# Kernel tuning notes

Hardware: AMD Instinct MI355X
Metric: run time of the kernel (lower is better)

Reference implementation:

```python
import jax, jax.numpy as jnp
import numpy as np

B = 4096
D_IN = 1024
H1 = 2048
H2 = 1024
E = 7          # num_experts, forced by broadcasting in source
T = 2          # num_tasks
NS = 7         # scene dimension of S
EMB_ROWS = 10
EMB_DIM = 16


def setup_inputs() -> dict:
    key = jax.random.key(0)
    ks = jax.random.split(key, 8)
    x = jax.random.normal(ks[0], (B, D_IN), dtype=jnp.float32)
    scene = jax.random.randint(ks[1], (B,), 0, E)
    # Expert MLP params, stacked over experts: Linear(D_IN->H1)+ReLU, Linear(H1->H2)+ReLU
    W1 = jax.random.normal(ks[2], (E, D_IN, H1), dtype=jnp.float32) * (1.0 / np.sqrt(D_IN))
    b1 = jnp.zeros((E, H1), dtype=jnp.float32)
    W2 = jax.random.normal(ks[3], (E, H1, H2), dtype=jnp.float32) * (1.0 / np.sqrt(H1))
    b2 = jnp.zeros((E, H2), dtype=jnp.float32)
    # Routing tensor S: [7, input_dim+16, num_experts] (xavier-like init)
    S = jax.random.normal(ks[4], (NS, D_IN + EMB_DIM, E), dtype=jnp.float32) * 0.02
    scene_emb = jax.random.normal(ks[5], (EMB_ROWS, EMB_DIM), dtype=jnp.float32)
    return {"x": x, "scene": scene, "W1": W1, "b1": b1, "W2": W2, "b2": b2,
            "S": S, "scene_emb": scene_emb}


def _forward(x, scene, W1, b1, W2, b2, S, scene_emb):
    # Experts (vectorized over the E expert MLPs): [B,E,H2]
    h = jax.nn.relu(jnp.einsum('bd,edh->beh', x, W1) + b1)
    experts_out = jax.nn.relu(jnp.einsum('beh,eho->beo', h, W2) + b2)

    se = scene_emb[scene]                       # [B,16]
    xc = jnp.concatenate([x, se], axis=-1)      # [B, D_IN+16]
    G = jnp.einsum('bd,sde->bse', xc, S)        # [B, 7, E]
    G = jnp.transpose(G, (0, 2, 1))             # [B, E, 7]
    G = jax.nn.softmax(G, axis=-1)

    logG = jnp.log(G)                           # [B, E, 7]
    q = jnp.sum(jnp.log(G * 7.0) / 7.0, axis=-1)  # [B, E]

    KG = jnp.eye(E, dtype=x.dtype)
    ses = KG[scene][:, None, :]                 # [B, 1, E]

    _, pi = jax.lax.top_k(jnp.sum(ses * logG, axis=-1), 6)  # [B,6]
    _, qi = jax.lax.top_k(q, 6)                              # [B,6]
    select = ((KG[pi].sum(axis=1) + KG[qi].sum(axis=1)) > 0).astype(x.dtype)  # [B,E]

    gate = jax.nn.softmax(jnp.sum(G * ses, axis=-1), axis=-1) * select  # [B,E]
    out = jnp.einsum('be,bed->bd', gate, experts_out)                    # [B,H2]
    # self.gate ModuleList is unused in the source forward; each task output is identical
    return jnp.stack([out] * T, axis=0)         # [T, B, H2]


def reference(x, scene, W1, b1, W2, b2, S, scene_emb):
    return _forward(x, scene, W1, b1, W2, b2, S, scene_emb)
```

## Files before the change

kernel.cpp:

```cpp
#include <hip/hip_runtime.h>
#include <hip/hip_bf16.h>

typedef unsigned short u16;
typedef __bf16 bf8 __attribute__((ext_vector_type(8)));
typedef float f4 __attribute__((ext_vector_type(4)));

__device__ __forceinline__ u16 f2bf(float f) {
    unsigned int u = __float_as_uint(f);
    u = (u + 0x7fffu + ((u >> 16) & 1u)) >> 16;
    return (u16)u;
}

__device__ __forceinline__ void gload16(const u16* g, u16* l) {
    __builtin_amdgcn_global_load_lds((const __attribute__((address_space(1))) void*)g,
                                     (__attribute__((address_space(3))) void*)l, 16, 0, 0);
}

__global__ void cvt_x_kernel(const float* __restrict__ in, u16* __restrict__ out, int n4) {
    int i = blockIdx.x * blockDim.x + threadIdx.x;
    int stride = gridDim.x * blockDim.x;
    for (; i < n4; i += stride) {
        float4 v = ((const float4*)in)[i];
        ushort4 o;
        o.x = f2bf(v.x); o.y = f2bf(v.y); o.z = f2bf(v.z); o.w = f2bf(v.w);
        ((ushort4*)out)[i] = o;
    }
}

__global__ void transpose_cvt_kernel(const float* __restrict__ in, u16* __restrict__ out,
                                     int R, int C) {
    __shared__ float t[32][33];
    int e = blockIdx.z;
    int c0 = blockIdx.x * 32, r0 = blockIdx.y * 32;
    int tx = threadIdx.x & 31, ty = threadIdx.x >> 5;
    const float* ip = in + (size_t)e * R * C;
    u16* op = out + (size_t)e * R * C;
#pragma unroll
    for (int k = 0; k < 32; k += 8)
        t[ty + k][tx] = ip[(size_t)(r0 + ty + k) * C + c0 + tx];
    __syncthreads();
#pragma unroll
    for (int k = 0; k < 32; k += 8)
        op[(size_t)(c0 + ty + k) * R + r0 + tx] = f2bf(t[tx][ty + k]);
}

__global__ void transpose_S_kernel(const float* __restrict__ S, float* __restrict__ ST) {
    int idx = blockIdx.x * 256 + threadIdx.x;
    if (idx >= 1040 * 52) return;
    int d = idx / 52, c = idx % 52;
    ST[idx] = (c < 49) ? S[(c / 7) * 7280 + d * 7 + (c % 7)] : 0.f;
}

__global__ void gating_kernel(const float* __restrict__ x, const int* __restrict__ scene,
                              const float* __restrict__ ST, const float* __restrict__ semb,
                              float* __restrict__ gate) {
    __shared__ float xc[4][1040];
    __shared__ float Lsh[4][49];
    int wv = threadIdx.x >> 6, lane = threadIdx.x & 63;
    int row = blockIdx.x * 4 + wv;
    float* xcw = xc[wv];
    const float* xr = x + (size_t)row * 1024;
    for (int d = lane; d < 1024; d += 64) xcw[d] = xr[d];
    int sc = scene[row];
    if (lane < 16) xcw[1024 + lane] = semb[sc * 16 + lane];
    __syncthreads();

    if (lane < 49) {
        const float* STp = ST + lane;
        float a0 = 0.f, a1 = 0.f, a2 = 0.f, a3 = 0.f;
        for (int d = 0; d < 1040; d += 4) {
            a0 += xcw[d]     * STp[d * 52];
            a1 += xcw[d + 1] * STp[d * 52 + 52];
            a2 += xcw[d + 2] * STp[d * 52 + 104];
            a3 += xcw[d + 3] * STp[d * 52 + 156];
        }
        Lsh[wv][lane] = (a0 + a1) + (a2 + a3);
    }
    __syncthreads();

    if (lane == 0) {
        float logG[7][7], Gsc[7], piS[7], qS[7];
        for (int e = 0; e < 7; e++) {
            float L[7];
            float m = -1e30f;
            for (int s = 0; s < 7; s++) { L[s] = Lsh[wv][s * 7 + e]; m = fmaxf(m, L[s]); }
            float sum = 0.f;
            for (int s = 0; s < 7; s++) sum += expf(L[s] - m);
            float lse = m + logf(sum);
            float qs = 0.f;
            for (int s = 0; s < 7; s++) { logG[e][s] = L[s] - lse; qs += logG[e][s]; }
            piS[e] = logG[e][sc];
            qS[e] = qs;
            Gsc[e] = expf(logG[e][sc]);
        }
        int epi = 0, eqi = 0; float bp = piS[0], bq = qS[0];
        for (int e = 1; e < 7; e++) {
            if (piS[e] <= bp) { bp = piS[e]; epi = e; }
            if (qS[e]  <= bq) { bq = qS[e];  eqi = e; }
        }
        float mg = -1e30f;
        for (int e = 0; e < 7; e++) mg = fmaxf(mg, Gsc[e]);
        float sum = 0.f;
        float ex[7];
        for (int e = 0; e < 7; e++) { ex[e] = expf(Gsc[e] - mg); sum += ex[e]; }
        float inv = 1.f / sum;
        for (int e = 0; e < 7; e++) {
            float g = ex[e] * inv;
            if (e == epi && e == eqi) g = 0.f;
            gate[row * 7 + e] = g;
        }
    }
}

__global__ __launch_bounds__(256, 2) void gemm1_kernel(
    const u16* __restrict__ A, const u16* __restrict__ BT,
    const float* __restrict__ b1, u16* __restrict__ H) {
    const int M = 4096, K = 1024, N = 2048;
    int e = blockIdx.z;
    int bm = blockIdx.y, bn = blockIdx.x;
    __shared__ __align__(16) u16 As[128 * 32];
    __shared__ __align__(16) u16 Bs[128 * 32];
    int tid = threadIdx.x, lane = tid & 63, w = tid >> 6;
    int wm = w >> 1, wn = w & 1;

    const u16* Ag = A + (size_t)(bm * 128 + (tid >> 2)) * K + (tid & 3) * 8;
    const u16* Bg = BT + (size_t)e * N * K + (size_t)(bn * 128 + (tid >> 2)) * K + (tid & 3) * 8;

    f4 acc[4][4] = {};
    int arow = lane & 15, kch = (lane >> 4) * 8;
    const u16* Asr = As + (wm * 64 + arow) * 32 + kch;
    const u16* Bsr = Bs + (wn * 64 + arow) * 32 + kch;

    for (int kt = 0; kt < K; kt += 32) {
        gload16(Ag + kt,           As + tid * 8);
        gload16(Ag + kt + 64 * K,  As + tid * 8 + 64 * 32);
        gload16(Bg + kt,           Bs + tid * 8);
        gload16(Bg + kt + 64 * K,  Bs + tid * 8 + 64 * 32);
        __syncthreads();
        bf8 a[4], b[4];
#pragma unroll
        for (int mi = 0; mi < 4; mi++) a[mi] = *(const bf8*)(Asr + mi * 16 * 32);
#pragma unroll
        for (int ni = 0; ni < 4; ni++) b[ni] = *(const bf8*)(Bsr + ni * 16 * 32);
#pragma unroll
        for (int mi = 0; mi < 4; mi++)
#pragma unroll
            for (int ni = 0; ni < 4; ni++)
                acc[mi][ni] = __builtin_amdgcn_mfma_f32_16x16x32_bf16(a[mi], b[ni], acc[mi][ni], 0, 0, 0);
        __syncthreads();
    }

    int cn0 = bn * 128 + wn * 64 + (lane & 15);
    int rm0 = bm * 128 + wm * 64 + (lane >> 4) * 4;
    float bias[4];
#pragma unroll
    for (int ni = 0; ni < 4; ni++) bias[ni] = b1[e * N + cn0 + ni * 16];
    u16* Hp = H + (size_t)e * M * N;
#pragma unroll
    for (int mi = 0; mi < 4; mi++)
#pragma unroll
        for (int i = 0; i < 4; i++) {
            size_t rbase = (size_t)(rm0 + mi * 16 + i) * N;
#pragma unroll
            for (int ni = 0; ni < 4; ni++) {
                float v = acc[mi][ni][i] + bias[ni];
                Hp[rbase + cn0 + ni * 16] = f2bf(fmaxf(v, 0.f));
            }
        }
}

__global__ __launch_bounds__(256, 2) void gemm2_kernel(
    const u16* __restrict__ H, const u16* __restrict__ W2T,
    const float* __restrict__ b2, const float* __restrict__ gate,
    float* __restrict__ part) {
    const int M = 4096, K = 2048, N = 1024;
    int id = blockIdx.x;
    int group = id >> 8;
    int id2 = id & 255;
    int bmr = id2 & 7, rest = id2 >> 3;
    int bn = rest >> 2, bmq = rest & 3;
    int bm = bmq * 8 + bmr;
    int e0 = group ? 4 : 0, e1 = group ? 7 : 4;

    __shared__ __align__(16) u16 As[128 * 32];
    __shared__ __align__(16) u16 Bs[128 * 32];
    __shared__ float gsh[128][7];
    int tid = threadIdx.x, lane = tid & 63, w = tid >> 6;
    int wm = w >> 1, wn = w & 1;

    for (int i = tid; i < 128 * 7; i += 256)
        gsh[i / 7][i % 7] = gate[(bm * 128 + i / 7) * 7 + i % 7];

    f4 fin[4][4] = {};
    int arow = lane & 15, kch = (lane >> 4) * 8;
    const u16* Asr = As + (wm * 64 + arow) * 32 + kch;
    const u16* Bsr = Bs + (wn * 64 + arow) * 32 + kch;
    int lrow0 = wm * 64 + (lane >> 4) * 4;
    int rm0 = bm * 128 + lrow0;
    int cn0 = bn * 128 + wn * 64 + (lane & 15);

    for (int e = e0; e < e1; e++) {
        const u16* Ag = H + ((size_t)e * M + bm * 128 + (tid >> 2)) * K + (tid & 3) * 8;
        const u16* Bg = W2T + ((size_t)e * N + bn * 128 + (tid >> 2)) * K + (tid & 3) * 8;
        f4 acc[4][4] = {};
        for (int kt = 0; kt < K; kt += 32) {
            gload16(Ag + kt,           As + tid * 8);
            gload16(Ag + kt + 64 * K,  As + tid * 8 + 64 * 32);
            gload16(Bg + kt,           Bs + tid * 8);
            gload16(Bg + kt + 64 * K,  Bs + tid * 8 + 64 * 32);
            __syncthreads();
            bf8 a[4], b[4];
#pragma unroll
            for (int mi = 0; mi < 4; mi++) a[mi] = *(const bf8*)(Asr + mi * 16 * 32);
#pragma unroll
            for (int ni = 0; ni < 4; ni++) b[ni] = *(const bf8*)(Bsr + ni * 16 * 32);
#pragma unroll
            for (int mi = 0; mi < 4; mi++)
#pragma unroll
                for (int ni = 0; ni < 4; ni++)
                    acc[mi][ni] = __builtin_amdgcn_mfma_f32_16x16x32_bf16(a[mi], b[ni], acc[mi][ni], 0, 0, 0);
            __syncthreads();
        }
        float bias[4];
#pragma unroll
        for (int ni = 0; ni < 4; ni++) bias[ni] = b2[e * N + cn0 + ni * 16];
#pragma unroll
        for (int mi = 0; mi < 4; mi++)
#pragma unroll
            for (int i = 0; i < 4; i++) {
                float g = gsh[lrow0 + mi * 16 + i][e];
#pragma unroll
                for (int ni = 0; ni < 4; ni++)
                    fin[mi][ni][i] += g * fmaxf(acc[mi][ni][i] + bias[ni], 0.f);
            }
    }

    float* po = part + (size_t)group * M * N;
#pragma unroll
    for (int mi = 0; mi < 4; mi++)
#pragma unroll
        for (int i = 0; i < 4; i++) {
            size_t r = (size_t)(rm0 + mi * 16 + i);
#pragma unroll
            for (int ni = 0; ni < 4; ni++)
                po[r * N + cn0 + ni * 16] = fin[mi][ni][i];
        }
}

__global__ void combine_kernel(const float* __restrict__ p0, const float* __restrict__ p1,
                               float* __restrict__ out, int n4) {
    int i = blockIdx.x * blockDim.x + threadIdx.x;
    int stride = gridDim.x * blockDim.x;
    for (; i < n4; i += stride) {
        float4 a = ((const float4*)p0)[i];
        float4 b = ((const float4*)p1)[i];
        float4 v = make_float4(a.x + b.x, a.y + b.y, a.z + b.z, a.w + b.w);
        ((float4*)out)[i] = v;
        ((float4*)out)[i + n4] = v;
    }
}

extern "C" void kernel_launch(void* const* d_in, const int* in_sizes, int n_in,
                              void* d_out, int out_size, void* d_ws, size_t ws_size,
                              hipStream_t stream) {
    const float* x     = (const float*)d_in[0];
    const int*   scene = (const int*)d_in[1];
    const float* W1    = (const float*)d_in[2];
    const float* b1    = (const float*)d_in[3];
    const float* W2    = (const float*)d_in[4];
    const float* b2    = (const float*)d_in[5];
    const float* S     = (const float*)d_in[6];
    const float* semb  = (const float*)d_in[7];
    float* out = (float*)d_out;

    char* ws = (char*)d_ws;
    float* part = (float*)(ws);
    u16*   xb   = (u16*)(ws);
    u16*   W1T  = (u16*)(ws + 8388608);
    u16*   W2T  = (u16*)(ws + 37748736);
    u16*   Hb   = (u16*)(ws + 67108864);
    float* gate = (float*)(ws + 184549376);
    float* ST   = (float*)(ws + 184664064);

    cvt_x_kernel<<<2048, 256, 0, stream>>>(x, xb, 4096 * 1024 / 4);
    transpose_cvt_kernel<<<dim3(64, 32, 7), 256, 0, stream>>>(W1, W1T, 1024, 2048);
    transpose_cvt_kernel<<<dim3(32, 64, 7), 256, 0, stream>>>(W2, W2T, 2048, 1024);
    transpose_S_kernel<<<(1040 * 52 + 255) / 256, 256, 0, stream>>>(S, ST);
    gating_kernel<<<1024, 256, 0, stream>>>(x, scene, ST, semb, gate);
    gemm1_kernel<<<dim3(16, 32, 7), 256, 0, stream>>>(xb, W1T, b1, Hb);
    gemm2_kernel<<<512, 256, 0, stream>>>(Hb, W2T, b2, gate, part);
    combine_kernel<<<2048, 256, 0, stream>>>(part, part + 4096 * 1024, out, 4096 * 1024 / 4);
}
```

Before: 425.0 us.

## Replace both expert GEMMs with double-buffered 8-wave 128x256 pipelined kernel

Replaces gemm1 and gemm2 with one templated 512-thread kernel. It uses 128x256 tiles with a K-step of 64, double-buffered LDS with an XOR swizzle, and interleaves async global-to-LDS loads with MFMA phases using explicit waitcnt, sched_barrier and setprio. The aim is to hide memory latency and cut the barrier and LDS bank-conflict overhead of the old single-buffered 128x128 loop. The gemm2 grid now uses 256 blocks with an XCD-aware mapping, which risks lower occupancy, and the hand-tuned waitcnt counts could be fragile.

```diff
diff --git a/kernel.cpp b/kernel.cpp
--- a/kernel.cpp
+++ b/kernel.cpp
@@ -112,139 +112,215 @@
     }
 }
 
-__global__ __launch_bounds__(256, 2) void gemm1_kernel(
-    const u16* __restrict__ A, const u16* __restrict__ BT,
-    const float* __restrict__ b1, u16* __restrict__ H) {
-    const int M = 4096, K = 1024, N = 2048;
-    int e = blockIdx.z;
-    int bm = blockIdx.y, bn = blockIdx.x;
-    __shared__ __align__(16) u16 As[128 * 32];
-    __shared__ __align__(16) u16 Bs[128 * 32];
-    int tid = threadIdx.x, lane = tid & 63, w = tid >> 6;
-    int wm = w >> 1, wn = w & 1;
-
-    const u16* Ag = A + (size_t)(bm * 128 + (tid >> 2)) * K + (tid & 3) * 8;
-    const u16* Bg = BT + (size_t)e * N * K + (size_t)(bn * 128 + (tid >> 2)) * K + (tid & 3) * 8;
+template<bool G2>
+__global__ __launch_bounds__(512, 2) void gemm8p_kernel(
+    const u16* __restrict__ Abase, const u16* __restrict__ Bbase,
+    const float* __restrict__ bias, const float* __restrict__ gate,
+    void* __restrict__ outp)
+{
+    constexpr int M = 4096;
+    constexpr int K = G2 ? 2048 : 1024;
+    constexpr int N = G2 ? 1024 : 2048;
+    constexpr int NT = K / 64;
+    constexpr int LOG2NT = G2 ? 5 : 4;
+
+    extern __shared__ u16 lds[];
+
+    const int tid = threadIdx.x;
+    const int lane = tid & 63;
+    const int wid = tid >> 6;
+    const int wr = wid >> 2, wc = wid & 3;
+    const int ln15 = lane & 15, lnk = (lane >> 4) * 8;
+
+    int bm, bn, e0, nE, grp;
+    if constexpr (G2) {
+        int id = blockIdx.x;
+        int xcd = id & 7, slot = id >> 3;
+        grp = xcd & 1;
+        bn = slot & 3;
+        bm = (slot >> 2) * 4 + (xcd >> 1);
+        e0 = grp * 4; nE = grp ? 3 : 4;
+    } else {
+        int id = blockIdx.x;
+        e0 = id >> 8;
+        bm = (id & 255) >> 3;
+        bn = id & 7;
+        nE = 1; grp = 0;
+    }
+    const int NTtot = nE * NT;
+
+    const int sr = tid >> 3;
+    const int sc = (tid & 7) * 8;
+
+    auto stageA = [&](int gt, int buf) {
+#pragma unroll
+        for (int l = 0; l < 2; ++l) {
+            int r = l * 64 + sr;
+            int cs = sc ^ (((r >> 2) & 1) << 4);
+            const u16* g = Abase + (G2 ? (size_t)(e0 + (gt >> LOG2NT)) * M * K : (size_t)0)
+                         + (size_t)(bm * 128 + r) * K + (gt & (NT - 1)) * 64 + cs;
+            gload16(g, lds + buf * 24576 + l * 4096 + tid * 8);
+        }
+    };
+    auto stageB = [&](int gt, int buf, int h) {
+#pragma unroll
+        for (int l = 0; l < 2; ++l) {
+            int rb = h * 128 + l * 64 + sr;
+            int cs = sc ^ (((rb >> 2) & 1) << 4);
+            const u16* g = Bbase + (size_t)(e0 + (gt >> LOG2NT)) * N * K
+                         + (size_t)(bn * 256 + rb) * K + (gt & (NT - 1)) * 64 + cs;
+            gload16(g, lds + buf * 24576 + 8192 + h * 8192 + l * 4096 + tid * 8);
+        }
+    };
+    auto aoff = [&](int mi, int ks) {
+        int r = wr * 64 + mi * 16 + ln15;
+        int c = ks * 32 + lnk;
+        return r * 64 + (c ^ (((r >> 2) & 1) << 4));
+    };
+    auto boff = [&](int ni, int ks) {
+        int rb = wc * 64 + ni * 16 + ln15;
+        int c = ks * 32 + lnk;
+        return rb * 64 + (c ^ (((rb >> 2) & 1) << 4));
+    };
 
     f4 acc[4][4] = {};
-    int arow = lane & 15, kch = (lane >> 4) * 8;
-    const u16* Asr = As + (wm * 64 + arow) * 32 + kch;
-    const u16* Bsr = Bs + (wn * 64 + arow) * 32 + kch;
-
-    for (int kt = 0; kt < K; kt += 32) {
-        gload16(Ag + kt,           As + tid * 8);
-        gload16(Ag + kt + 64 * K,  As + tid * 8 + 64 * 32);
-        gload16(Bg + kt,           Bs + tid * 8);
-        gload16(Bg + kt + 64 * K,  Bs + tid * 8 + 64 * 32);
-        __syncthreads();
-        bf8 a[4], b[4];
-#pragma unroll
-        for (int mi = 0; mi < 4; mi++) a[mi] = *(const bf8*)(Asr + mi * 16 * 32);
-#pragma unroll
-        for (int ni = 0; ni < 4; ni++) b[ni] = *(const bf8*)(Bsr + ni * 16 * 32);
-#pragma unroll
-        for (int mi = 0; mi < 4; mi++)
-#pragma unroll
-            for (int ni = 0; ni < 4; ni++)
-                acc[mi][ni] = __builtin_amdgcn_mfma_f32_16x16x32_bf16(a[mi], b[ni], acc[mi][ni], 0, 0, 0);
-        __syncthreads();
-    }
-
-    int cn0 = bn * 128 + wn * 64 + (lane & 15);
-    int rm0 = bm * 128 + wm * 64 + (lane >> 4) * 4;
-    float bias[4];
-#pragma unroll
-    for (int ni = 0; ni < 4; ni++) bias[ni] = b1[e * N + cn0 + ni * 16];
-    u16* Hp = H + (size_t)e * M * N;
-#pragma unroll
-    for (int mi = 0; mi < 4; mi++)
-#pragma unroll
-        for (int i = 0; i < 4; i++) {
-            size_t rbase = (size_t)(rm0 + mi * 16 + i) * N;
-#pragma unroll
-            for (int ni = 0; ni < 4; ni++) {
-                float v = acc[mi][ni][i] + bias[ni];
-                Hp[rbase + cn0 + ni * 16] = f2bf(fmaxf(v, 0.f));
+    f4 fin[4][4] = {};
+    bf8 aA[2][2], bL[2][2], bH[2][2];
+
+    stageA(0, 0); stageB(0, 0, 0); stageB(0, 0, 1);
+
+    for (int gt = 0; gt < NTtot; ++gt) {
+        const int cur = gt & 1, nxt = cur ^ 1;
+        const bool more = (gt + 1 < NTtot);
+        const u16* Ac = lds + cur * 24576;
+        const u16* Bc = lds + cur * 24576 + 8192;
+        if (more) {
+            stageA(gt + 1, nxt); stageB(gt + 1, nxt, 0);
+            asm volatile("s_waitcnt vmcnt(4)" ::: "memory");
+        } else {
+            asm volatile("s_waitcnt vmcnt(0)" ::: "memory");
+        }
+        __builtin_amdgcn_sched_barrier(0);
+        __builtin_amdgcn_s_barrier();
+        __builtin_amdgcn_sched_barrier(0);
+#pragma unroll
+        for (int mi = 0; mi < 2; ++mi)
+#pragma unroll
+            for (int ks = 0; ks < 2; ++ks)
+                aA[mi][ks] = *(const bf8*)(Ac + aoff(mi, ks));
+#pragma unroll
+        for (int ni = 0; ni < 2; ++ni)
+#pragma unroll
+            for (int ks = 0; ks < 2; ++ks)
+                bL[ni][ks] = *(const bf8*)(Bc + boff(ni, ks));
+        asm volatile("s_waitcnt lgkmcnt(0)" ::: "memory");
+        __builtin_amdgcn_sched_barrier(0);
+        __builtin_amdgcn_s_setprio(1);
+#pragma unroll
+        for (int mi = 0; mi < 2; ++mi)
+#pragma unroll
+            for (int ni = 0; ni < 2; ++ni)
+#pragma unroll
+                for (int ks = 0; ks < 2; ++ks)
+                    acc[mi][ni] = __builtin_amdgcn_mfma_f32_16x16x32_bf16(aA[mi][ks], bL[ni][ks], acc[mi][ni], 0, 0, 0);
+        __builtin_amdgcn_s_setprio(0);
+        if (more) stageB(gt + 1, nxt, 1);
+#pragma unroll
+        for (int ni = 0; ni < 2; ++ni)
+#pragma unroll
+            for (int ks = 0; ks < 2; ++ks)
+                bH[ni][ks] = *(const bf8*)(Bc + boff(2 + ni, ks));
+        asm volatile("s_waitcnt lgkmcnt(0)" ::: "memory");
+        __builtin_amdgcn_sched_barrier(0);
+        __builtin_amdgcn_s_setprio(1);
+#pragma unroll
+        for (int mi = 0; mi < 2; ++mi)
+#pragma unroll
+            for (int ni = 0; ni < 2; ++ni)
+#pragma unroll
+                for (int ks = 0; ks < 2; ++ks)
+                    acc[mi][2 + ni] = __builtin_amdgcn_mfma_f32_16x16x32_bf16(aA[mi][ks], bH[ni][ks], acc[mi][2 + ni], 0, 0, 0);
+        __builtin_amdgcn_s_setprio(0);
+#pragma unroll
+        for (int mi = 0; mi < 2; ++mi)
+#pragma unroll
+            for (int ks = 0; ks < 2; ++ks)
+                aA[mi][ks] = *(const bf8*)(Ac + aoff(2 + mi, ks));
+        asm volatile("s_waitcnt lgkmcnt(0)" ::: "memory");
+        __builtin_amdgcn_sched_barrier(0);
+        __builtin_amdgcn_s_setprio(1);
+#pragma unroll
+        for (int mi = 0; mi < 2; ++mi)
+#pragma unroll
+            for (int ni = 0; ni < 2; ++ni)
+#pragma unroll
+                for (int ks = 0; ks < 2; ++ks)
+                    acc[2 + mi][2 + ni] = __builtin_amdgcn_mfma_f32_16x16x32_bf16(aA[mi][ks], bH[ni][ks], acc[2 + mi][2 + ni], 0, 0, 0);
+        __builtin_amdgcn_s_setprio(0);
+        __builtin_amdgcn_sched_barrier(0);
+        __builtin_amdgcn_s_barrier();
+        __builtin_amdgcn_sched_barrier(0);
+        __builtin_amdgcn_s_setprio(1);
+#pragma unroll
+        for (int mi = 0; mi < 2; ++mi)
+#pragma unroll
+            for (int ni = 0; ni < 2; ++ni)
+#pragma unroll
+                for (int ks = 0; ks < 2; ++ks)
+                    acc[2 + mi][ni] = __builtin_amdgcn_mfma_f32_16x16x32_bf16(aA[mi][ks], bL[ni][ks], acc[2 + mi][ni], 0, 0, 0);
+        __builtin_amdgcn_s_setprio(0);
+        __builtin_amdgcn_sched_barrier(0);
+        if constexpr (G2) {
+            if ((gt & (NT - 1)) == NT - 1) {
+                int e = e0 + (gt >> LOG2NT);
+                float bloc[4];
+#pragma unroll
+                for (int ni = 0; ni < 4; ++ni)
+                    bloc[ni] = bias[e * N + bn * 256 + wc * 64 + ni * 16 + ln15];
+#pragma unroll
+                for (int mi = 0; mi < 4; ++mi)
+#pragma unroll
+                    for (int i = 0; i < 4; ++i) {
+                        int row = bm * 128 + wr * 64 + mi * 16 + (lane >> 4) * 4 + i;
+                        float g = gate[row * 7 + e];
+#pragma unroll
+                        for (int ni = 0; ni < 4; ++ni) {
+                            fin[mi][ni][i] += g * fmaxf(acc[mi][ni][i] + bloc[ni], 0.f);
+                            acc[mi][ni][i] = 0.f;
+                        }
+                    }
             }
         }
-}
-
-__global__ __launch_bounds__(256, 2) void gemm2_kernel(
-    const u16* __restrict__ H, const u16* __restrict__ W2T,
-    const float* __restrict__ b2, const float* __restrict__ gate,
-    float* __restrict__ part) {
-    const int M = 4096, K = 2048, N = 1024;
-    int id = blockIdx.x;
-    int group = id >> 8;
-    int id2 = id & 255;
-    int bmr = id2 & 7, rest = id2 >> 3;
-    int bn = rest >> 2, bmq = rest & 3;
-    int bm = bmq * 8 + bmr;
-    int e0 = group ? 4 : 0, e1 = group ? 7 : 4;
-
-    __shared__ __align__(16) u16 As[128 * 32];
-    __shared__ __align__(16) u16 Bs[128 * 32];
-    __shared__ float gsh[128][7];
-    int tid = threadIdx.x, lane = tid & 63, w = tid >> 6;
-    int wm = w >> 1, wn = w & 1;
-
-    for (int i = tid; i < 128 * 7; i += 256)
-        gsh[i / 7][i % 7] = gate[(bm * 128 + i / 7) * 7 + i % 7];
-
-    f4 fin[4][4] = {};
-    int arow = lane & 15, kch = (lane >> 4) * 8;
-    const u16* Asr = As + (wm * 64 + arow) * 32 + kch;
-    const u16* Bsr = Bs + (wn * 64 + arow) * 32 + kch;
-    int lrow0 = wm * 64 + (lane >> 4) * 4;
-    int rm0 = bm * 128 + lrow0;
-    int cn0 = bn * 128 + wn * 64 + (lane & 15);
-
-    for (int e = e0; e < e1; e++) {
-        const u16* Ag = H + ((size_t)e * M + bm * 128 + (tid >> 2)) * K + (tid & 3) * 8;
-        const u16* Bg = W2T + ((size_t)e * N + bn * 128 + (tid >> 2)) * K + (tid & 3) * 8;
-        f4 acc[4][4] = {};
-        for (int kt = 0; kt < K; kt += 32) {
-            gload16(Ag + kt,           As + tid * 8);
-            gload16(Ag + kt + 64 * K,  As + tid * 8 + 64 * 32);
-            gload16(Bg + kt,           Bs + tid * 8);
-            gload16(Bg + kt + 64 * K,  Bs + tid * 8 + 64 * 32);
-            __syncthreads();
-            bf8 a[4], b[4];
-#pragma unroll
-            for (int mi = 0; mi < 4; mi++) a[mi] = *(const bf8*)(Asr + mi * 16 * 32);
-#pragma unroll
-            for (int ni = 0; ni < 4; ni++) b[ni] = *(const bf8*)(Bsr + ni * 16 * 32);
-#pragma unroll
-            for (int mi = 0; mi < 4; mi++)
-#pragma unroll
-                for (int ni = 0; ni < 4; ni++)
-                    acc[mi][ni] = __builtin_amdgcn_mfma_f32_16x16x32_bf16(a[mi], b[ni], acc[mi][ni], 0, 0, 0);
-            __syncthreads();
-        }
-        float bias[4];
-#pragma unroll
-        for (int ni = 0; ni < 4; ni++) bias[ni] = b2[e * N + cn0 + ni * 16];
-#pragma unroll
-        for (int mi = 0; mi < 4; mi++)
-#pragma unroll
-            for (int i = 0; i < 4; i++) {
-                float g = gsh[lrow0 + mi * 16 + i][e];
-#pragma unroll
-                for (int ni = 0; ni < 4; ni++)
-                    fin[mi][ni][i] += g * fmaxf(acc[mi][ni][i] + bias[ni], 0.f);
+    }
+
+    if constexpr (G2) {
+        float* po = (float*)outp + (size_t)grp * M * N;
+#pragma unroll
+        for (int mi = 0; mi < 4; ++mi)
+#pragma unroll
+            for (int i = 0; i < 4; ++i) {
+                size_t row = (size_t)(bm * 128 + wr * 64 + mi * 16 + (lane >> 4) * 4 + i);
+#pragma unroll
+                for (int ni = 0; ni < 4; ++ni)
+                    po[row * N + bn * 256 + wc * 64 + ni * 16 + ln15] = fin[mi][ni][i];
             }
-    }
-
-    float* po = part + (size_t)group * M * N;
-#pragma unroll
-    for (int mi = 0; mi < 4; mi++)
-#pragma unroll
-        for (int i = 0; i < 4; i++) {
-            size_t r = (size_t)(rm0 + mi * 16 + i);
-#pragma unroll
-            for (int ni = 0; ni < 4; ni++)
-                po[r * N + cn0 + ni * 16] = fin[mi][ni][i];
-        }
+    } else {
+        float bloc[4];
+#pragma unroll
+        for (int ni = 0; ni < 4; ++ni)
+            bloc[ni] = bias[e0 * N + bn * 256 + wc * 64 + ni * 16 + ln15];
+        u16* Hp = (u16*)outp + (size_t)e0 * M * N;
+#pragma unroll
+        for (int mi = 0; mi < 4; ++mi)
+#pragma unroll
+            for (int i = 0; i < 4; ++i) {
+                size_t row = (size_t)(bm * 128 + wr * 64 + mi * 16 + (lane >> 4) * 4 + i);
+#pragma unroll
+                for (int ni = 0; ni < 4; ++ni)
+                    Hp[row * N + bn * 256 + wc * 64 + ni * 16 + ln15] =
+                        f2bf(fmaxf(acc[mi][ni][i] + bloc[ni], 0.f));
+            }
+    }
 }
 
 __global__ void combine_kernel(const float* __restrict__ p0, const float* __restrict__ p1,
@@ -282,12 +358,17 @@
     float* gate = (float*)(ws + 184549376);
     float* ST   = (float*)(ws + 184664064);
 
+    (void)hipFuncSetAttribute(reinterpret_cast<const void*>(gemm8p_kernel<false>),
+                              hipFuncAttributeMaxDynamicSharedMemorySize, 98304);
+    (void)hipFuncSetAttribute(reinterpret_cast<const void*>(gemm8p_kernel<true>),
+                              hipFuncAttributeMaxDynamicSharedMemorySize, 98304);
+
     cvt_x_kernel<<<2048, 256, 0, stream>>>(x, xb, 4096 * 1024 / 4);
     transpose_cvt_kernel<<<dim3(64, 32, 7), 256, 0, stream>>>(W1, W1T, 1024, 2048);
     transpose_cvt_kernel<<<dim3(32, 64, 7), 256, 0, stream>>>(W2, W2T, 2048, 1024);
     transpose_S_kernel<<<(1040 * 52 + 255) / 256, 256, 0, stream>>>(S, ST);
     gating_kernel<<<1024, 256, 0, stream>>>(x, scene, ST, semb, gate);
-    gemm1_kernel<<<dim3(16, 32, 7), 256, 0, stream>>>(xb, W1T, b1, Hb);
-    gemm2_kernel<<<512, 256, 0, stream>>>(Hb, W2T, b2, gate, part);
+    gemm8p_kernel<false><<<1792, 512, 98304, stream>>>(xb, W1T, b1, nullptr, Hb);
+    gemm8p_kernel<true><<<256, 512, 98304, stream>>>(Hb, W2T, b2, gate, part);
     combine_kernel<<<2048, 256, 0, stream>>>(part, part + 4096 * 1024, out, 4096 * 1024 / 4);
 }
```

After: 402.9 us. 1.05x faster.
